# Kernel tuning notes

Measured on AMD Instinct MI355X. Metric: run time of the kernel, lower is better.

## Reference

```python
import jax, jax.numpy as jnp
import numpy as np

G = 128          # voxel grid side
R = 2048         # rays
S = 128          # samples per ray
VD = 28          # 1 density + 27 SH coeffs (3 channels x 9)

# SH constants (match source module)
Y00 = 0.5 * np.sqrt(1.0 / np.pi)
H3 = 0.5 * np.sqrt(3.0 / np.pi)
H15 = 0.5 * np.sqrt(15.0 / np.pi)
Q5 = 0.25 * np.sqrt(5.0 / np.pi)
Q15 = 0.25 * np.sqrt(15.0 / np.pi)


def setup_inputs() -> dict:
    key = jax.random.key(0)
    k1, k2, k3, k4 = jax.random.split(key, 4)
    grid = jax.random.uniform(k1, (G, G, G, VD), dtype=jnp.float32)
    # continuous positions strictly inside the grid so all 8 corners are valid
    sample_positions = jax.random.uniform(k2, (R, S, 3), dtype=jnp.float32) * (G - 2)
    sample_distances = jax.random.uniform(k3, (R, S), dtype=jnp.float32) * 0.05
    ang = jax.random.uniform(k4, (R, 2), dtype=jnp.float32)
    viewing_angles = ang * jnp.array([np.pi, 2.0 * np.pi], dtype=jnp.float32)
    return {"grid": grid, "sample_positions": sample_positions,
            "sample_distances": sample_distances, "viewing_angles": viewing_angles}


def sh_basis(viewing_angles):
    # order matches harmonic(): [C00, Cm11, C01, C11, Cm22, Cm12, C02, C12, C22]
    th, ph = viewing_angles[:, 0], viewing_angles[:, 1]
    st, ct = jnp.sin(th), jnp.cos(th)
    sp, cp = jnp.sin(ph), jnp.cos(ph)
    return jnp.stack([
        jnp.full_like(th, Y00),          # Y_0_0
        H3 * st * sp,                    # Y_m1_1
        H3 * ct,                         # Y_0_1
        H3 * st * cp,                    # Y_1_1
        H15 * st * cp * st * sp,         # Y_m2_2
        H15 * st * sp * ct,              # Y_m1_2
        Q5 * (3.0 * ct * ct - 1.0),      # Y_0_2
        H15 * st * cp * ct,              # Y_1_2
        Q15 * ((st * cp) ** 2 - (st * sp) ** 2),  # Y_2_2
    ], axis=-1)  # [R, 9]


def trilinear(grid, pos):
    # pos: [R, S, 3] continuous coords -> [R, S, VD]
    p0 = jnp.floor(pos).astype(jnp.int32)
    fd = pos - p0.astype(pos.dtype)                  # fractional offsets (x_d, y_d, z_d)
    gmax = jnp.int32(grid.shape[0] - 1)
    out = jnp.zeros(pos.shape[:-1] + (grid.shape[-1],), dtype=grid.dtype)
    for dx in (0, 1):
        wx = fd[..., 0] if dx else (1.0 - fd[..., 0])
        for dy in (0, 1):
            wy = fd[..., 1] if dy else (1.0 - fd[..., 1])
            for dz in (0, 1):
                wz = fd[..., 2] if dz else (1.0 - fd[..., 2])
                ix = jnp.clip(p0[..., 0] + dx, 0, gmax)
                iy = jnp.clip(p0[..., 1] + dy, 0, gmax)
                iz = jnp.clip(p0[..., 2] + dz, 0, gmax)
                out = out + (wx * wy * wz)[..., None] * grid[ix, iy, iz]
    return out


def reference(grid, sample_positions, sample_distances, viewing_angles):
    feats = trilinear(grid, sample_positions)          # [R, S, 28]
    sigma = feats[..., 0]                              # [R, S]
    coeffs = feats[..., 1:].reshape(feats.shape[0], feats.shape[1], 3, 9)
    att = jnp.exp(-sigma * sample_distances)           # exp(-sigma_j * d_j)
    # Faithful to source: transmittance[i] = sum_{j<=i} exp(-sigma_j d_j)
    trans = jnp.cumsum(att, axis=1)                    # inclusive cumsum
    weight = trans * (1.0 - att)                       # [R, S]
    Y = sh_basis(viewing_angles)                       # [R, 9]
    rgb = jnp.einsum('rscn,rn->rsc', coeffs, Y)        # [R, S, 3]
    return jnp.sum(weight[..., None] * rgb, axis=1)    # [R, 3]
```

## Files before the change

### kernel.cpp

```cpp
#include <hip/hip_runtime.h>

#define GDIM 128
#define NS   128
#define VD   28

__global__ __launch_bounds__(512, 4) void plenoxel_kernel(
    const float* __restrict__ grid,
    const float* __restrict__ pos,
    const float* __restrict__ dist,
    const float* __restrict__ ang,
    float* __restrict__ out)
{
    const int r   = blockIdx.x;
    const int tid = threadIdx.x;
    const int s   = tid & (NS - 1);
    const int p   = tid >> 7;
    const int dx  = p >> 1;
    const int dy  = p & 1;
    const int lane = tid & 63;

    const float th = ang[2 * r + 0];
    const float ph = ang[2 * r + 1];
    float st, ct, sp, cp;
    sincosf(th, &st, &ct);
    sincosf(ph, &sp, &cp);
    const float Y00 = 0.28209479177387814f;
    const float H3  = 0.4886025119029199f;
    const float H15 = 1.0925484305920792f;
    const float Q5  = 0.31539156525252005f;
    const float Q15 = 0.5462742152960396f;
    float Y[9];
    Y[0] = Y00;
    Y[1] = H3 * st * sp;
    Y[2] = H3 * ct;
    Y[3] = H3 * st * cp;
    Y[4] = H15 * (st * cp) * (st * sp);
    Y[5] = H15 * (st * sp) * ct;
    Y[6] = Q5 * (3.f * ct * ct - 1.f);
    Y[7] = H15 * (st * cp) * ct;
    Y[8] = Q15 * ((st * cp) * (st * cp) - (st * sp) * (st * sp));

    const float* pp = pos + ((size_t)r * NS + s) * 3;
    const float x = pp[0], y = pp[1], z = pp[2];
    const float fx0 = floorf(x), fy0 = floorf(y), fz0 = floorf(z);
    const float fx = x - fx0, fy = y - fy0, fz = z - fz0;
    const int jx  = min(max((int)fx0 + dx, 0), GDIM - 1);
    const int jy  = min(max((int)fy0 + dy, 0), GDIM - 1);
    const int jz0 = min(max((int)fz0,      0), GDIM - 1);
    const int jz1 = min(max((int)fz0 + 1,  0), GDIM - 1);

    const float wxy = (dx ? fx : 1.f - fx) * (dy ? fy : 1.f - fy);
    const float wz0 = wxy * (1.f - fz);
    const float wz1 = wxy * fz;

    const float4* g0 = (const float4*)(grid + (((size_t)jx * GDIM + jy) * GDIM + jz0) * VD);
    const float4* g1 = (const float4*)(grid + (((size_t)jx * GDIM + jy) * GDIM + jz1) * VD);

    float f0[28], f1[28];
#pragma unroll
    for (int j = 0; j < 7; ++j) ((float4*)f0)[j] = g0[j];
#pragma unroll
    for (int j = 0; j < 7; ++j) ((float4*)f1)[j] = g1[j];

    float psig = wz0 * f0[0] + wz1 * f1[0];
    float d0r = 0.f, d0g = 0.f, d0b = 0.f;
    float d1r = 0.f, d1g = 0.f, d1b = 0.f;
#pragma unroll
    for (int n = 0; n < 9; ++n) {
        d0r += f0[1 + n]  * Y[n];
        d0g += f0[10 + n] * Y[n];
        d0b += f0[19 + n] * Y[n];
        d1r += f1[1 + n]  * Y[n];
        d1g += f1[10 + n] * Y[n];
        d1b += f1[19 + n] * Y[n];
    }
    const float pr = wz0 * d0r + wz1 * d1r;
    const float pg = wz0 * d0g + wz1 * d1g;
    const float pb = wz0 * d0b + wz1 * d1b;

    __shared__ float4 part[512];
    part[tid] = make_float4(psig, pr, pg, pb);
    __syncthreads();

    __shared__ float wave0_total;
    __shared__ float fin[2][3];

    float t = 0.f, att = 0.f, rr = 0.f, rg = 0.f, rb = 0.f;
    if (tid < NS) {
        const float4 a = part[s];
        const float4 b = part[s + 128];
        const float4 c = part[s + 256];
        const float4 e = part[s + 384];
        const float sigma = a.x + b.x + c.x + e.x;
        rr = a.y + b.y + c.y + e.y;
        rg = a.z + b.z + c.z + e.z;
        rb = a.w + b.w + c.w + e.w;

        const float d = dist[(size_t)r * NS + s];
        att = expf(-sigma * d);

        t = att;
#pragma unroll
        for (int o = 1; o < 64; o <<= 1) {
            const float v = __shfl_up(t, (unsigned)o, 64);
            if (lane >= o) t += v;
        }
        if (tid == 63) wave0_total = t;
    }
    __syncthreads();

    if (tid < NS) {
        const float trans  = t + (tid >= 64 ? wave0_total : 0.f);
        const float weight = trans * (1.f - att);
        float a0 = weight * rr, a1 = weight * rg, a2 = weight * rb;
#pragma unroll
        for (int o = 32; o > 0; o >>= 1) {
            a0 += __shfl_down(a0, (unsigned)o, 64);
            a1 += __shfl_down(a1, (unsigned)o, 64);
            a2 += __shfl_down(a2, (unsigned)o, 64);
        }
        if (lane == 0) {
            const int wv = tid >> 6;
            fin[wv][0] = a0; fin[wv][1] = a1; fin[wv][2] = a2;
        }
    }
    __syncthreads();
    if (tid == 0) {
        out[(size_t)r * 3 + 0] = fin[0][0] + fin[1][0];
        out[(size_t)r * 3 + 1] = fin[0][1] + fin[1][1];
        out[(size_t)r * 3 + 2] = fin[0][2] + fin[1][2];
    }
}

extern "C" void kernel_launch(void* const* d_in, const int* in_sizes, int n_in,
                              void* d_out, int out_size, void* d_ws, size_t ws_size,
                              hipStream_t stream) {
    const float* grid = (const float*)d_in[0];
    const float* pos  = (const float*)d_in[1];
    const float* dst  = (const float*)d_in[2];
    const float* ang  = (const float*)d_in[3];
    float* out = (float*)d_out;

    const int R = in_sizes[3] / 2;
    plenoxel_kernel<<<R, 512, 0, stream>>>(grid, pos, dst, ang, out);
}
```

Before: 370.3 us.

## Interleave corner lanes per sample and reduce with shuffles instead of LDS

Sample-to-thread mapping changes so the four xy-corner threads of one sample are adjacent lanes. Their partials are combined with xor shuffles rather than an LDS staging array. The cumulative transmittance scan then runs across all eight waves, with per-wave carries in shared memory, replacing the old single-pass scan in two waves. This removes one LDS round trip and the serialized tail in which only 128 threads worked. The trade-off is that each thread's two z-corner loads now hit different cells from its neighbours, which changes the gather access pattern.

```diff
diff --git a/kernel.cpp b/kernel.cpp
--- a/kernel.cpp
+++ b/kernel.cpp
@@ -11,13 +11,14 @@
     const float* __restrict__ ang,
     float* __restrict__ out)
 {
-    const int r   = blockIdx.x;
-    const int tid = threadIdx.x;
-    const int s   = tid & (NS - 1);
-    const int p   = tid >> 7;
-    const int dx  = p >> 1;
-    const int dy  = p & 1;
+    const int r    = blockIdx.x;
+    const int tid  = threadIdx.x;
+    const int s    = tid >> 2;
+    const int p    = tid & 3;
+    const int dx   = p >> 1;
+    const int dy   = p & 1;
     const int lane = tid & 63;
+    const int wv   = tid >> 6;
 
     const float th = ang[2 * r + 0];
     const float ph = ang[2 * r + 1];
@@ -74,61 +75,55 @@
         d1g += f1[10 + n] * Y[n];
         d1b += f1[19 + n] * Y[n];
     }
-    const float pr = wz0 * d0r + wz1 * d1r;
-    const float pg = wz0 * d0g + wz1 * d1g;
-    const float pb = wz0 * d0b + wz1 * d1b;
+    float pr = wz0 * d0r + wz1 * d1r;
+    float pg = wz0 * d0g + wz1 * d1g;
+    float pb = wz0 * d0b + wz1 * d1b;
 
-    __shared__ float4 part[512];
-    part[tid] = make_float4(psig, pr, pg, pb);
+#pragma unroll
+    for (int o = 1; o <= 2; o <<= 1) {
+        psig += __shfl_xor(psig, (unsigned)o, 64);
+        pr   += __shfl_xor(pr,   (unsigned)o, 64);
+        pg   += __shfl_xor(pg,   (unsigned)o, 64);
+        pb   += __shfl_xor(pb,   (unsigned)o, 64);
+    }
+
+    const float d   = dist[(size_t)r * NS + s];
+    const float att = expf(-psig * d);
+
+    float t = att;
+#pragma unroll
+    for (int o = 4; o < 64; o <<= 1) {
+        const float v = __shfl_up(t, (unsigned)o, 64);
+        if (lane >= o) t += v;
+    }
+
+    __shared__ float wave_sum[8];
+    __shared__ float fin[8][3];
+    if (lane == 63) wave_sum[wv] = t;
+    __syncthreads();
+    float carry = 0.f;
+#pragma unroll
+    for (int w = 0; w < 8; ++w) carry += (w < wv) ? wave_sum[w] : 0.f;
+
+    const float trans  = t + carry;
+    const float weight = trans * (1.f - att);
+
+    const float m = (p == 0) ? weight : 0.f;
+    float a0 = m * pr, a1 = m * pg, a2 = m * pb;
+#pragma unroll
+    for (int o = 4; o < 64; o <<= 1) {
+        a0 += __shfl_xor(a0, (unsigned)o, 64);
+        a1 += __shfl_xor(a1, (unsigned)o, 64);
+        a2 += __shfl_xor(a2, (unsigned)o, 64);
+    }
+    if (lane == 0) { fin[wv][0] = a0; fin[wv][1] = a1; fin[wv][2] = a2; }
     __syncthreads();
 
-    __shared__ float wave0_total;
-    __shared__ float fin[2][3];
-
-    float t = 0.f, att = 0.f, rr = 0.f, rg = 0.f, rb = 0.f;
-    if (tid < NS) {
-        const float4 a = part[s];
-        const float4 b = part[s + 128];
-        const float4 c = part[s + 256];
-        const float4 e = part[s + 384];
-        const float sigma = a.x + b.x + c.x + e.x;
-        rr = a.y + b.y + c.y + e.y;
-        rg = a.z + b.z + c.z + e.z;
-        rb = a.w + b.w + c.w + e.w;
-
-        const float d = dist[(size_t)r * NS + s];
-        att = expf(-sigma * d);
-
-        t = att;
+    if (tid < 3) {
+        float acc = 0.f;
 #pragma unroll
-        for (int o = 1; o < 64; o <<= 1) {
-            const float v = __shfl_up(t, (unsigned)o, 64);
-            if (lane >= o) t += v;
-        }
-        if (tid == 63) wave0_total = t;
-    }
-    __syncthreads();
-
-    if (tid < NS) {
-        const float trans  = t + (tid >= 64 ? wave0_total : 0.f);
-        const float weight = trans * (1.f - att);
-        float a0 = weight * rr, a1 = weight * rg, a2 = weight * rb;
-#pragma unroll
-        for (int o = 32; o > 0; o >>= 1) {
-            a0 += __shfl_down(a0, (unsigned)o, 64);
-            a1 += __shfl_down(a1, (unsigned)o, 64);
-            a2 += __shfl_down(a2, (unsigned)o, 64);
-        }
-        if (lane == 0) {
-            const int wv = tid >> 6;
-            fin[wv][0] = a0; fin[wv][1] = a1; fin[wv][2] = a2;
-        }
-    }
-    __syncthreads();
-    if (tid == 0) {
-        out[(size_t)r * 3 + 0] = fin[0][0] + fin[1][0];
-        out[(size_t)r * 3 + 1] = fin[0][1] + fin[1][1];
-        out[(size_t)r * 3 + 2] = fin[0][2] + fin[1][2];
+        for (int w = 0; w < 8; ++w) acc += fin[w][tid];
+        out[(size_t)r * 3 + tid] = acc;
     }
 }
 
```

Result: no change. 370.4 us (+0.0%).
